# Kernel optimization log

Measured on AMD Instinct MI355X. Metric: run time of the kernel, lower is better.

The kernel has to match this reference:

```python
import jax, jax.numpy as jnp
import numpy as np

N_NODES = 50000
N_HOPS = 4
N_EDGES = 800000
NFEAT = 512
HIDDEN = 512
NCLASS = 128
ATT_HID = 64


def setup_inputs() -> dict:
    key = jax.random.key(0)
    ks = jax.random.split(key, 12)
    s = lambda *sh: 1.0 / np.sqrt(sh[0])
    inp = {}
    inp['x'] = jax.random.normal(ks[0], (N_NODES, NFEAT), dtype=jnp.float32)
    inp['W1'] = jax.random.normal(ks[1], (NFEAT, HIDDEN), dtype=jnp.float32) * s(NFEAT)
    inp['W2'] = jax.random.normal(ks[2], (HIDDEN, NCLASS), dtype=jnp.float32) * s(HIDDEN)
    inp['b2'] = jax.random.normal(ks[3], (NCLASS,), dtype=jnp.float32) * 0.01
    inp['Wg'] = jax.random.normal(ks[4], (NCLASS, NCLASS), dtype=jnp.float32) * s(NCLASS)
    inp['Wa'] = jax.random.normal(ks[5], (2 * NCLASS, ATT_HID), dtype=jnp.float32) * s(2 * NCLASS)
    inp['ba'] = jax.random.normal(ks[6], (ATT_HID,), dtype=jnp.float32) * 0.01
    inp['va'] = jax.random.normal(ks[7], (ATT_HID,), dtype=jnp.float32) * s(ATT_HID)
    inp['adj_values'] = jax.random.uniform(ks[8], (N_HOPS, N_EDGES), dtype=jnp.float32)
    inp['adj_indices'] = jax.random.randint(ks[9], (N_HOPS, 2, N_EDGES), 0, N_NODES, dtype=jnp.int32)
    inp['idx'] = jnp.arange(N_NODES, dtype=jnp.int32)
    return inp


def reference(x, W1, W2, b2, Wg, Wa, ba, va, adj_values, adj_indices, idx):
    # x: [N, nfeat] -> relu(linear1) -> linear2 : [N, C]
    z = jax.nn.relu(x @ W1) @ W2 + b2  # [N, C]
    anchor = z[idx]                    # [Na, C]
    na = idx.shape[0]
    n_hops = adj_indices.shape[0]
    embs = [anchor]
    for h in range(n_hops):  # fixed small structural loop over hops
        rows = adj_indices[h, 0]  # destination anchor row per edge
        cols = adj_indices[h, 1]  # source node per edge
        # sparse matmul: agg[r] = sum_e v_e * z[cols_e]  (LayerConvol)
        agg = jax.ops.segment_sum(adj_values[h][:, None] * z[cols], rows, num_segments=na)
        embs.append(agg @ Wg)  # [Na, C]
    seq = jnp.stack(embs, axis=1)  # [Na, H+1, C]
    # AttenMlp: additive attention of anchor query over hop embeddings
    q = jnp.broadcast_to(anchor[:, None, :], seq.shape)       # [Na, H+1, C]
    feat = jnp.concatenate([q, seq], axis=-1)                 # [Na, H+1, 2C]
    scores = jnp.tanh(feat @ Wa + ba) @ va                    # [Na, H+1]
    alpha = jax.nn.softmax(scores, axis=1)
    out = jnp.einsum('nh,nhc->nc', alpha, seq)                # [Na, C]
    return jax.nn.log_softmax(out, axis=1)
```

## Files before the change

### kernel.cpp

```cpp
#include <hip/hip_runtime.h>

#define NA    50000
#define NFEAT 512
#define HID   512
#define NC    128
#define AH    64
#define NE    800000
#define NHOP  4
#define NBUCK 196
#define CAPB  5120

typedef __bf16 bf16x8 __attribute__((ext_vector_type(8)));
typedef float  f32x4  __attribute__((ext_vector_type(4)));

__device__ __forceinline__ unsigned short f2bf(float f){
  union { float f; unsigned u; } a; a.f = f;
  return (unsigned short)((a.u + 0x7fffu + ((a.u >> 16) & 1u)) >> 16);
}
__device__ __forceinline__ float bf2f(unsigned short h){
  union { unsigned u; float f; } a; a.u = ((unsigned)h) << 16;
  return a.f;
}
__device__ __forceinline__ float uasf(unsigned u){
  union { unsigned u; float f; } a; a.u = u;
  return a.f;
}
__device__ __forceinline__ float tanh_fast(float x){
  x = fminf(15.f, fmaxf(-15.f, x));
  float e = __expf(2.f * x);
  return (e - 1.f) / (e + 1.f);
}

__device__ __forceinline__ void g2l16(const void* g, void* l){
  __builtin_amdgcn_global_load_lds(
      (const __attribute__((address_space(1))) void*)g,
      (__attribute__((address_space(3))) void*)l, 16, 0, 0);
}


__global__ void cast_x_kernel(const float* __restrict__ in, unsigned short* __restrict__ out, int n4){
  int i = blockIdx.x * 256 + threadIdx.x;
  if (i >= n4) return;
  float4 v = reinterpret_cast<const float4*>(in)[i];
  ushort4 o; o.x = f2bf(v.x); o.y = f2bf(v.y); o.z = f2bf(v.z); o.w = f2bf(v.w);
  reinterpret_cast<ushort4*>(out)[i] = o;
}

__global__ void prep_kernel(const float* __restrict__ W1, const float* __restrict__ W2,
                            const float* __restrict__ Wg, const float* __restrict__ Wa,
                            unsigned short* __restrict__ W1T, unsigned short* __restrict__ W2T,
                            unsigned short* __restrict__ WgT, unsigned short* __restrict__ WaT,
                            unsigned short* __restrict__ WfuseT){
  const int b = blockIdx.x, tid = threadIdx.x;
  if (b < 1024){
    int i = b * 256 + tid;
    int n = i >> 9, k = i & 511;
    W1T[i] = f2bf(W1[(size_t)k * HID + n]);
  } else if (b < 1280){
    int i = (b - 1024) * 256 + tid;
    int n = i >> 9, k = i & 511;
    W2T[i] = f2bf(W2[(size_t)k * NC + n]);
  } else if (b < 1344){
    int i = (b - 1280) * 256 + tid;
    int n = i >> 7, k = i & 127;
    WgT[i] = f2bf(Wg[(size_t)k * NC + n]);
  } else if (b < 1408){
    int i = (b - 1344) * 256 + tid;
    int n = i >> 7, k = i & 127;
    float v = (n < 64) ? Wa[(size_t)k * AH + n] : Wa[(size_t)(128 + k) * AH + (n - 64)];
    WaT[i] = f2bf(v);
  } else {
    int i = (b - 1408) * 256 + tid;
    int j = i >> 7, n = i & 127;
    float s = 0.f;
    for (int k = 0; k < 128; k++)
      s += Wa[(size_t)(128 + k) * AH + j] * Wg[(size_t)n * 128 + k];
    WfuseT[i] = f2bf(s);
  }
}

template<int OP, int SWZ>
__global__ __launch_bounds__(256) void gemm_bt(
    const unsigned short* __restrict__ A, const unsigned short* __restrict__ BT,
    unsigned short* __restrict__ Cb, const float* __restrict__ bias,
    int M, int N, int K)
{
  int row0, col0;
  if (SWZ){
    const int xcd = blockIdx.x & 7, slot = blockIdx.x >> 3;
    const int r = xcd * 49 + (slot >> 2);
    if (r >= 391) return;
    row0 = r * 128; col0 = (slot & 3) * 128;
  } else {
    row0 = blockIdx.x * 128; col0 = blockIdx.y * 128;
  }
  __shared__ unsigned short As[128 * 32];
  __shared__ unsigned short Bs[128 * 32];
  const int tid = threadIdx.x;
  const int wave = tid >> 6, lane = tid & 63;
  const int wr = (wave >> 1) * 64, wc = (wave & 1) * 64;
  f32x4 acc[4][4];
  #pragma unroll
  for (int m = 0; m < 4; m++)
    #pragma unroll
    for (int n = 0; n < 4; n++) acc[m][n] = (f32x4){0.f, 0.f, 0.f, 0.f};
  const int lrow = lane >> 2, lk = (lane & 3) * 8;

  for (int k0 = 0; k0 < K; k0 += 32){
    __syncthreads();
    #pragma unroll
    for (int j = 0; j < 2; j++){
      const int rb = (wave * 2 + j) * 16;
      const int ra = rb + lrow;
      int gr = row0 + ra; gr = gr < M ? gr : M - 1;
      g2l16(A + (size_t)gr * K + k0 + lk, As + rb * 32);
      int gc = col0 + ra; gc = gc < N ? gc : N - 1;
      g2l16(BT + (size_t)gc * K + k0 + lk, Bs + rb * 32);
    }
    __syncthreads();
    bf16x8 af[4], bfr[4];
    #pragma unroll
    for (int m = 0; m < 4; m++)
      af[m] = *reinterpret_cast<const bf16x8*>(&As[(wr + m * 16 + (lane & 15)) * 32 + (lane >> 4) * 8]);
    #pragma unroll
    for (int n = 0; n < 4; n++)
      bfr[n] = *reinterpret_cast<const bf16x8*>(&Bs[(wc + n * 16 + (lane & 15)) * 32 + (lane >> 4) * 8]);
    #pragma unroll
    for (int m = 0; m < 4; m++)
      #pragma unroll
      for (int n = 0; n < 4; n++)
        acc[m][n] = __builtin_amdgcn_mfma_f32_16x16x32_bf16(af[m], bfr[n], acc[m][n], 0, 0, 0);
  }

  const int rbase = row0 + wr + (lane >> 4) * 4;
  const int cbase = col0 + wc + (lane & 15);
  #pragma unroll
  for (int m = 0; m < 4; m++){
    #pragma unroll
    for (int n = 0; n < 4; n++){
      const int col = cbase + n * 16;
      #pragma unroll
      for (int i = 0; i < 4; i++){
        const int row = rbase + m * 16 + i;
        if (row < M && col < N){
          float v = acc[m][n][i];
          if (OP == 0){ v = v > 0.f ? v : 0.f; }
          else        { v += bias[col]; }
          Cb[(size_t)row * N + col] = f2bf(v);
        }
      }
    }
  }
}

__global__ __launch_bounds__(256) void gemm_sweep(
    const unsigned short* __restrict__ aggbf, const unsigned short* __restrict__ zbf,
    const unsigned short* __restrict__ WgT, const unsigned short* __restrict__ WfuseT,
    const unsigned short* __restrict__ WaT,
    unsigned short* __restrict__ embs, unsigned short* __restrict__ EW, float* __restrict__ ZW)
{
  const int zi = blockIdx.z;
  const unsigned short* A; const unsigned short* BT;
  unsigned short* Cb = nullptr; float* Cf = nullptr; int N;
  if (zi < 4)      { A = aggbf + (size_t)zi * NA * NC;       BT = WgT;    Cb = embs + (size_t)zi * NA * NC; N = 128; }
  else if (zi < 8) { A = aggbf + (size_t)(zi - 4) * NA * NC; BT = WfuseT; Cb = EW + (size_t)(zi - 4) * NA * AH; N = 64; }
  else             { A = zbf;                                BT = WaT;    Cf = ZW; N = 128; }

  __shared__ unsigned short As[128 * 32];
  __shared__ unsigned short Bs[128 * 32];
  const int tid = threadIdx.x;
  const int wave = tid >> 6, lane = tid & 63;
  const int row0 = blockIdx.x * 128;
  const int wr = (wave >> 1) * 64, wc = (wave & 1) * 64;
  f32x4 acc[4][4];
  #pragma unroll
  for (int m = 0; m < 4; m++)
    #pragma unroll
    for (int n = 0; n < 4; n++) acc[m][n] = (f32x4){0.f, 0.f, 0.f, 0.f};

  for (int k0 = 0; k0 < 128; k0 += 32){
    __syncthreads();
    #pragma unroll
    for (int j = 0; j < 2; j++){
      const int rb = (wave * 2 + j) * 16;
      int gr = row0 + rb + (lane >> 2); gr = gr < NA ? gr : NA - 1;
      g2l16(A + (size_t)gr * 128 + k0 + (lane & 3) * 8, As + rb * 32);
      int gc = rb + (lane >> 2); gc = gc < N ? gc : N - 1;
      g2l16(BT + (size_t)gc * 128 + k0 + (lane & 3) * 8, Bs + rb * 32);
    }
    __syncthreads();
    bf16x8 bfr[4];
    #pragma unroll
    for (int n = 0; n < 4; n++)
      bfr[n] = *reinterpret_cast<const bf16x8*>(&Bs[(wc + n * 16 + (lane & 15)) * 32 + (lane >> 4) * 8]);
    #pragma unroll
    for (int m = 0; m < 4; m++){
      bf16x8 a = *reinterpret_cast<const bf16x8*>(&As[(wr + m * 16 + (lane & 15)) * 32 + (lane >> 4) * 8]);
      #pragma unroll
      for (int n = 0; n < 4; n++)
        acc[m][n] = __builtin_amdgcn_mfma_f32_16x16x32_bf16(a, bfr[n], acc[m][n], 0, 0, 0);
    }
  }

  const int rbase = row0 + wr + (lane >> 4) * 4;
  const int cbase = wc + (lane & 15);
  #pragma unroll
  for (int m = 0; m < 4; m++){
    #pragma unroll
    for (int n = 0; n < 4; n++){
      const int col = cbase + n * 16;
      #pragma unroll
      for (int i = 0; i < 4; i++){
        const int row = rbase + m * 16 + i;
        if (row < NA && col < N){
          float v = acc[m][n][i];
          if (Cf) Cf[(size_t)row * N + col] = v;
          else    Cb[(size_t)row * N + col] = f2bf(v);
        }
      }
    }
  }
}

__global__ __launch_bounds__(256) void binA_kernel(
    const int* __restrict__ adji, const float* __restrict__ adjv,
    int* __restrict__ fill, long long* __restrict__ binned)
{
  const int h = blockIdx.y, tid = threadIdx.x;
  const int e0 = blockIdx.x * 2048;
  __shared__ int lhist[NBUCK], lbase[NBUCK], lfill[NBUCK];
  for (int i = tid; i < NBUCK; i += 256){ lhist[i] = 0; lfill[i] = 0; }
  __syncthreads();
  int rr[8]; unsigned hh[8]; float vv[8];
  #pragma unroll
  for (int k = 0; k < 8; k++){
    int e = e0 + k * 256 + tid;
    bool ok = e < NE;
    int r = ok ? adji[(size_t)h * 2 * NE + e] : -1;
    int c = ok ? adji[(size_t)h * 2 * NE + NE + e] : 0;
    vv[k] = ok ? adjv[(size_t)h * NE + e] : 0.f;
    rr[k] = r;
    hh[k] = ((unsigned)(r & 255) << 17) | (unsigned)c;
    if (ok) atomicAdd(&lhist[r >> 8], 1);
  }
  __syncthreads();
  if (tid < NBUCK) lbase[tid] = atomicAdd(&fill[h * NBUCK + tid], lhist[tid]);
  __syncthreads();
  #pragma unroll
  for (int k = 0; k < 8; k++){
    if (rr[k] >= 0){
      int b = rr[k] >> 8;
      int p = lbase[b] + atomicAdd(&lfill[b], 1);
      if (p < CAPB)
        binned[((size_t)(h * NBUCK + b)) * CAPB + p] =
            ((long long)hh[k] << 32) | (unsigned)__float_as_int(vv[k]);
    }
  }
}

__global__ __launch_bounds__(1024) void bscan_kernel(const int* __restrict__ fill,
                                                     int* __restrict__ bbase, int* __restrict__ offs){
  __shared__ int tmp[1024];
  int tid = threadIdx.x;
  int v = (tid < NHOP * NBUCK) ? fill[tid] : 0;
  tmp[tid] = v; __syncthreads();
  for (int o = 1; o < 1024; o <<= 1){
    int t = (tid >= o) ? tmp[tid - o] : 0;
    __syncthreads();
    tmp[tid] += t;
    __syncthreads();
  }
  if (tid < NHOP * NBUCK) bbase[tid] = tmp[tid] - v;
  if (tid == 0) offs[NHOP * NA] = NHOP * NE;
}

__global__ __launch_bounds__(256) void binB_kernel(
    const int* __restrict__ fill, const int* __restrict__ bbase,
    const long long* __restrict__ binned,
    int* __restrict__ offs, long long* __restrict__ pvc)
{
  const int b = blockIdx.x, h = blockIdx.y, tid = threadIdx.x;
  const int hb = h * NBUCK + b;
  const int cnt = min(fill[hb], CAPB);
  const long long* src = binned + (size_t)hb * CAPB;
  const int gbase = bbase[hb];
  const int rowbase = b << 8;
  const int nrows = min(256, NA - rowbase);
  __shared__ long long sdata[CAPB];
  __shared__ int lhist[256], lpre[256], lfill2[256];
  lhist[tid] = 0; lfill2[tid] = 0;
  __syncthreads();
  for (int p = tid; p < cnt; p += 256)
    atomicAdd(&lhist[(unsigned)(src[p] >> 32) >> 17], 1);
  __syncthreads();
  int v = lhist[tid]; lpre[tid] = v; __syncthreads();
  for (int o = 1; o < 256; o <<= 1){
    int t = (tid >= o) ? lpre[tid - o] : 0;
    __syncthreads();
    lpre[tid] += t;
    __syncthreads();
  }
  int excl = lpre[tid] - v;
  if (tid < nrows) offs[h * NA + rowbase + tid] = gbase + excl;
  lpre[tid] = excl;
  __syncthreads();
  for (int p = tid; p < cnt; p += 256){
    long long rec = src[p];
    unsigned hi = (unsigned)(rec >> 32);
    int lr = hi >> 17;
    long long out = (rec & 0xffffffffLL) | ((long long)(hi & 0x1ffffu) << 32);
    int pos = lpre[lr] + atomicAdd(&lfill2[lr], 1);
    if (pos < CAPB) sdata[pos] = out;
    else            pvc[(size_t)gbase + pos] = out;
  }
  __syncthreads();
  for (int p = tid; p < cnt; p += 256)
    pvc[(size_t)gbase + p] = sdata[p];
}

#define GR 4
__global__ __launch_bounds__(256) void gather_kernel(
    const int* __restrict__ offs, const long long* __restrict__ pvc,
    const unsigned short* __restrict__ zbf, unsigned short* __restrict__ aggbf)
{
  const int h = blockIdx.y;
  const int w = threadIdx.x >> 6, lane = threadIdx.x & 63;
  const int row = blockIdx.x * GR + w;
  const int base = h * NA + row;
  const int s = offs[base], e = offs[base + 1];
  __shared__ alignas(16) long long srec[GR][64];
  const unsigned* z32 = (const unsigned*)zbf;
  const int4* sr2 = (const int4*)&srec[w][0];
  float a0 = 0.f, a1 = 0.f, b0 = 0.f, b1 = 0.f;
  for (int p0 = s; p0 < e; p0 += 64){
    long long r = 0;
    if (p0 + lane < e) r = __builtin_nontemporal_load(&pvc[p0 + lane]);
    srec[w][lane] = r;
    const int quads = (min(64, e - p0) + 3) >> 2;
    #pragma unroll 4
    for (int q = 0; q < quads; q++){
      int4 ra = sr2[2 * q], rb = sr2[2 * q + 1];
      unsigned z0 = z32[((unsigned)ra.y << 6) + lane];
      unsigned z1 = z32[((unsigned)ra.w << 6) + lane];
      unsigned z2 = z32[((unsigned)rb.y << 6) + lane];
      unsigned z3 = z32[((unsigned)rb.w << 6) + lane];
      float v0 = uasf((unsigned)ra.x), v1 = uasf((unsigned)ra.z);
      float v2 = uasf((unsigned)rb.x), v3 = uasf((unsigned)rb.z);
      a0 += v0 * uasf(z0 << 16); a1 += v0 * uasf(z0 & 0xffff0000u);
      b0 += v1 * uasf(z1 << 16); b1 += v1 * uasf(z1 & 0xffff0000u);
      a0 += v2 * uasf(z2 << 16); a1 += v2 * uasf(z2 & 0xffff0000u);
      b0 += v3 * uasf(z3 << 16); b1 += v3 * uasf(z3 & 0xffff0000u);
    }
  }
  ushort2 o; o.x = f2bf(a0 + b0); o.y = f2bf(a1 + b1);
  *reinterpret_cast<ushort2*>(aggbf + (size_t)base * NC + lane * 2) = o;
}

__global__ __launch_bounds__(256) void final_kernel(
    const unsigned short* __restrict__ zbf, const unsigned short* __restrict__ embs,
    const float* __restrict__ ZW, const unsigned short* __restrict__ EW,
    const float* __restrict__ ba, const float* __restrict__ va,
    const int* __restrict__ idx, float* __restrict__ out)
{
  int tid = threadIdx.x, wave = tid >> 6, lane = tid & 63;
  int n = blockIdx.x * 4 + wave;
  if (n >= NA) return;
  int an = idx[n];
  float qa = ZW[(size_t)an * NC + lane] + ba[lane];
  float vaj = va[lane];
  float sc[5];
  {
    float s0 = ZW[(size_t)an * NC + 64 + lane];
    float t = tanh_fast(qa + s0) * vaj;
    #pragma unroll
    for (int o = 32; o; o >>= 1) t += __shfl_xor(t, o);
    sc[0] = t;
  }
  #pragma unroll
  for (int h = 1; h < 5; h++){
    float sh = bf2f(EW[((size_t)(h - 1) * NA + n) * AH + lane]);
    float t = tanh_fast(qa + sh) * vaj;
    #pragma unroll
    for (int o = 32; o; o >>= 1) t += __shfl_xor(t, o);
    sc[h] = t;
  }
  float m = sc[0];
  #pragma unroll
  for (int h = 1; h < 5; h++) m = fmaxf(m, sc[h]);
  float al[5], den = 0.f;
  #pragma unroll
  for (int h = 0; h < 5; h++){ al[h] = __expf(sc[h] - m); den += al[h]; }
  float inv = 1.f / den;
  float o0 = al[0] * bf2f(zbf[(size_t)an * NC + lane]);
  float o1 = al[0] * bf2f(zbf[(size_t)an * NC + 64 + lane]);
  #pragma unroll
  for (int h = 1; h < 5; h++){
    o0 += al[h] * bf2f(embs[((size_t)(h - 1) * NA + n) * NC + lane]);
    o1 += al[h] * bf2f(embs[((size_t)(h - 1) * NA + n) * NC + 64 + lane]);
  }
  o0 *= inv; o1 *= inv;
  float mx = fmaxf(o0, o1);
  #pragma unroll
  for (int o = 32; o; o >>= 1) mx = fmaxf(mx, __shfl_xor(mx, o));
  float se = __expf(o0 - mx) + __expf(o1 - mx);
  #pragma unroll
  for (int o = 32; o; o >>= 1) se += __shfl_xor(se, o);
  float ls = __logf(se);
  out[(size_t)n * NC + lane]      = o0 - mx - ls;
  out[(size_t)n * NC + 64 + lane] = o1 - mx - ls;
}


extern "C" void kernel_launch(void* const* d_in, const int* in_sizes, int n_in,
                              void* d_out, int out_size, void* d_ws, size_t ws_size,
                              hipStream_t stream)
{
  const float* x    = (const float*)d_in[0];
  const float* W1   = (const float*)d_in[1];
  const float* W2   = (const float*)d_in[2];
  const float* b2   = (const float*)d_in[3];
  const float* Wg   = (const float*)d_in[4];
  const float* Wa   = (const float*)d_in[5];
  const float* ba   = (const float*)d_in[6];
  const float* va   = (const float*)d_in[7];
  const float* adjv = (const float*)d_in[8];
  const int*   adji = (const int*)d_in[9];
  const int*   idx  = (const int*)d_in[10];
  float* out = (float*)d_out;
  (void)in_sizes; (void)n_in; (void)out_size; (void)ws_size;

  char* w = (char*)d_ws;
  auto alloc = [&](size_t b) -> char* { char* p = w; w += (b + 255) & ~(size_t)255; return p; };
  unsigned short* Scr1 = (unsigned short*)alloc((size_t)NA * NFEAT * 2);
  unsigned short* Hbuf = (unsigned short*)alloc((size_t)NA * HID * 2);
  unsigned short* W1T  = (unsigned short*)alloc((size_t)HID * NFEAT * 2);
  unsigned short* W2T  = (unsigned short*)alloc((size_t)NC * HID * 2);
  unsigned short* WgT  = (unsigned short*)alloc((size_t)NC * NC * 2);
  unsigned short* WaT  = (unsigned short*)alloc((size_t)NC * NC * 2);
  unsigned short* WfuseT = (unsigned short*)alloc((size_t)AH * NC * 2);
  unsigned short* zbf  = (unsigned short*)alloc((size_t)NA * NC * 2);
  float*          ZW   = (float*)alloc((size_t)NA * NC * 4);
  int* fill  = (int*)alloc((size_t)NHOP * NBUCK * 4);
  int* bbase = (int*)alloc((size_t)NHOP * NBUCK * 4);
  int* offs  = (int*)alloc(((size_t)NHOP * NA + 1) * 4);
  long long* pvc = (long long*)alloc((size_t)NHOP * NE * 8);
  unsigned short* Xbf   = Scr1;
  long long* binned     = (long long*)Scr1;
  unsigned short* embs  = Scr1;
  unsigned short* aggbf = Hbuf;
  unsigned short* EW    = (unsigned short*)pvc;

  cast_x_kernel<<<dim3((NA * NFEAT / 4 + 255) / 256), 256, 0, stream>>>(x, Xbf, NA * NFEAT / 4);
  prep_kernel<<<dim3(1440), 256, 0, stream>>>(W1, W2, Wg, Wa, W1T, W2T, WgT, WaT, WfuseT);

  gemm_bt<0, 1><<<dim3(1568, 1, 1), 256, 0, stream>>>(Xbf, W1T, Hbuf, nullptr, NA, HID, NFEAT);
  gemm_bt<1, 0><<<dim3(391, 1, 1), 256, 0, stream>>>(Hbuf, W2T, zbf, b2, NA, NC, HID);

  hipMemsetAsync(fill, 0, (size_t)NHOP * NBUCK * 4, stream);
  binA_kernel<<<dim3((NE + 2047) / 2048, NHOP), 256, 0, stream>>>(adji, adjv, fill, binned);
  bscan_kernel<<<dim3(1), 1024, 0, stream>>>(fill, bbase, offs);
  binB_kernel<<<dim3(NBUCK, NHOP), 256, 0, stream>>>(fill, bbase, binned, offs, pvc);

  gather_kernel<<<dim3(NA / GR, NHOP), 256, 0, stream>>>(offs, pvc, zbf, aggbf);
  gemm_sweep<<<dim3(391, 1, 9), 256, 0, stream>>>(aggbf, zbf, WgT, WfuseT, WaT, embs, EW, ZW);

  final_kernel<<<dim3(NA / 4), 256, 0, stream>>>(zbf, embs, ZW, EW, ba, va, idx, out);
}
```

Before: 341.2 us.

## Store ZW in bf16, retile EW gemm, premultiply gather indices, fold memset

Several small changes land together. The ZW projection is now stored as bf16 instead of fp32, which halves its write and read traffic. The EW slices of gemm_sweep use 256-row tiles with all waves covering the full 64 columns instead of wasting half the tile, and the source indices in pvc are pre-shifted by 6 so the gather skips a shift per load. The fill memset is folded into prep_kernel to save one launch. The risks are bf16 rounding on the attention scores, and the pre-shift must still fit in the packed 32 bits.

Result: no change. 337.2 us (-1.2%).

```diff
diff --git a/kernel.cpp b/kernel.cpp
--- a/kernel.cpp
+++ b/kernel.cpp
@@ -50,7 +50,7 @@
                             const float* __restrict__ Wg, const float* __restrict__ Wa,
                             unsigned short* __restrict__ W1T, unsigned short* __restrict__ W2T,
                             unsigned short* __restrict__ WgT, unsigned short* __restrict__ WaT,
-                            unsigned short* __restrict__ WfuseT){
+                            unsigned short* __restrict__ WfuseT, int* __restrict__ fill){
   const int b = blockIdx.x, tid = threadIdx.x;
   if (b < 1024){
     int i = b * 256 + tid;
@@ -69,13 +69,16 @@
     int n = i >> 7, k = i & 127;
     float v = (n < 64) ? Wa[(size_t)k * AH + n] : Wa[(size_t)(128 + k) * AH + (n - 64)];
     WaT[i] = f2bf(v);
-  } else {
+  } else if (b < 1440){
     int i = (b - 1408) * 256 + tid;
     int j = i >> 7, n = i & 127;
     float s = 0.f;
     for (int k = 0; k < 128; k++)
       s += Wa[(size_t)(128 + k) * AH + j] * Wg[(size_t)n * 128 + k];
     WfuseT[i] = f2bf(s);
+  } else {
+    int i = (b - 1440) * 256 + tid;
+    if (i < NHOP * NBUCK) fill[i] = 0;
   }
 }
 
@@ -157,36 +160,54 @@
     const unsigned short* __restrict__ aggbf, const unsigned short* __restrict__ zbf,
     const unsigned short* __restrict__ WgT, const unsigned short* __restrict__ WfuseT,
     const unsigned short* __restrict__ WaT,
-    unsigned short* __restrict__ embs, unsigned short* __restrict__ EW, float* __restrict__ ZW)
+    unsigned short* __restrict__ embs, unsigned short* __restrict__ EW,
+    unsigned short* __restrict__ ZWb)
 {
   const int zi = blockIdx.z;
-  const unsigned short* A; const unsigned short* BT;
-  unsigned short* Cb = nullptr; float* Cf = nullptr; int N;
+  const bool ew = (zi >= 4 && zi < 8);
+  const int row0 = blockIdx.x * (ew ? 256 : 128);
+  if (row0 >= NA) return;
+  const unsigned short* A; const unsigned short* BT; unsigned short* Cb; int N;
   if (zi < 4)      { A = aggbf + (size_t)zi * NA * NC;       BT = WgT;    Cb = embs + (size_t)zi * NA * NC; N = 128; }
-  else if (zi < 8) { A = aggbf + (size_t)(zi - 4) * NA * NC; BT = WfuseT; Cb = EW + (size_t)(zi - 4) * NA * AH; N = 64; }
-  else             { A = zbf;                                BT = WaT;    Cf = ZW; N = 128; }
-
-  __shared__ unsigned short As[128 * 32];
+  else if (ew)     { A = aggbf + (size_t)(zi - 4) * NA * NC; BT = WfuseT; Cb = EW + (size_t)(zi - 4) * NA * AH; N = 64; }
+  else             { A = zbf;                                BT = WaT;    Cb = ZWb; N = 128; }
+
+  __shared__ unsigned short As[256 * 32];
   __shared__ unsigned short Bs[128 * 32];
   const int tid = threadIdx.x;
   const int wave = tid >> 6, lane = tid & 63;
-  const int row0 = blockIdx.x * 128;
-  const int wr = (wave >> 1) * 64, wc = (wave & 1) * 64;
+  const int wr = ew ? wave * 64 : (wave >> 1) * 64;
+  const int wc = ew ? 0 : (wave & 1) * 64;
   f32x4 acc[4][4];
   #pragma unroll
   for (int m = 0; m < 4; m++)
     #pragma unroll
     for (int n = 0; n < 4; n++) acc[m][n] = (f32x4){0.f, 0.f, 0.f, 0.f};
+  const int lrow = lane >> 2, lk = (lane & 3) * 8;
 
   for (int k0 = 0; k0 < 128; k0 += 32){
     __syncthreads();
-    #pragma unroll
-    for (int j = 0; j < 2; j++){
-      const int rb = (wave * 2 + j) * 16;
-      int gr = row0 + rb + (lane >> 2); gr = gr < NA ? gr : NA - 1;
-      g2l16(A + (size_t)gr * 128 + k0 + (lane & 3) * 8, As + rb * 32);
-      int gc = rb + (lane >> 2); gc = gc < N ? gc : N - 1;
-      g2l16(BT + (size_t)gc * 128 + k0 + (lane & 3) * 8, Bs + rb * 32);
+    if (ew){
+      #pragma unroll
+      for (int j = 0; j < 4; j++){
+        const int rb = (wave * 4 + j) * 16;
+        int gr = row0 + rb + lrow; gr = gr < NA ? gr : NA - 1;
+        g2l16(A + (size_t)gr * 128 + k0 + lk, As + rb * 32);
+      }
+      {
+        const int rb = wave * 16;
+        int gc = rb + lrow; gc = gc < 64 ? gc : 63;
+        g2l16(BT + (size_t)gc * 128 + k0 + lk, Bs + rb * 32);
+      }
+    } else {
+      #pragma unroll
+      for (int j = 0; j < 2; j++){
+        const int rb = (wave * 2 + j) * 16;
+        int gr = row0 + rb + lrow; gr = gr < NA ? gr : NA - 1;
+        g2l16(A + (size_t)gr * 128 + k0 + lk, As + rb * 32);
+        int gc = rb + lrow; gc = gc < N ? gc : N - 1;
+        g2l16(BT + (size_t)gc * 128 + k0 + lk, Bs + rb * 32);
+      }
     }
     __syncthreads();
     bf16x8 bfr[4];
@@ -212,11 +233,8 @@
       #pragma unroll
       for (int i = 0; i < 4; i++){
         const int row = rbase + m * 16 + i;
-        if (row < NA && col < N){
-          float v = acc[m][n][i];
-          if (Cf) Cf[(size_t)row * N + col] = v;
-          else    Cb[(size_t)row * N + col] = f2bf(v);
-        }
+        if (row < NA && col < N)
+          Cb[(size_t)row * N + col] = f2bf(acc[m][n][i]);
       }
     }
   }
@@ -308,7 +326,7 @@
     long long rec = src[p];
     unsigned hi = (unsigned)(rec >> 32);
     int lr = hi >> 17;
-    long long out = (rec & 0xffffffffLL) | ((long long)(hi & 0x1ffffu) << 32);
+    long long out = (rec & 0xffffffffLL) | ((long long)((hi & 0x1ffffu) << 6) << 32);
     int pos = lpre[lr] + atomicAdd(&lfill2[lr], 1);
     if (pos < CAPB) sdata[pos] = out;
     else            pvc[(size_t)gbase + pos] = out;
@@ -340,10 +358,10 @@
     #pragma unroll 4
     for (int q = 0; q < quads; q++){
       int4 ra = sr2[2 * q], rb = sr2[2 * q + 1];
-      unsigned z0 = z32[((unsigned)ra.y << 6) + lane];
-      unsigned z1 = z32[((unsigned)ra.w << 6) + lane];
-      unsigned z2 = z32[((unsigned)rb.y << 6) + lane];
-      unsigned z3 = z32[((unsigned)rb.w << 6) + lane];
+      unsigned z0 = z32[(unsigned)ra.y + lane];
+      unsigned z1 = z32[(unsigned)ra.w + lane];
+      unsigned z2 = z32[(unsigned)rb.y + lane];
+      unsigned z3 = z32[(unsigned)rb.w + lane];
       float v0 = uasf((unsigned)ra.x), v1 = uasf((unsigned)ra.z);
       float v2 = uasf((unsigned)rb.x), v3 = uasf((unsigned)rb.z);
       a0 += v0 * uasf(z0 << 16); a1 += v0 * uasf(z0 & 0xffff0000u);
@@ -358,7 +376,7 @@
 
 __global__ __launch_bounds__(256) void final_kernel(
     const unsigned short* __restrict__ zbf, const unsigned short* __restrict__ embs,
-    const float* __restrict__ ZW, const unsigned short* __restrict__ EW,
+    const unsigned short* __restrict__ ZWb, const unsigned short* __restrict__ EW,
     const float* __restrict__ ba, const float* __restrict__ va,
     const int* __restrict__ idx, float* __restrict__ out)
 {
@@ -366,11 +384,11 @@
   int n = blockIdx.x * 4 + wave;
   if (n >= NA) return;
   int an = idx[n];
-  float qa = ZW[(size_t)an * NC + lane] + ba[lane];
+  float qa = bf2f(ZWb[(size_t)an * NC + lane]) + ba[lane];
   float vaj = va[lane];
   float sc[5];
   {
-    float s0 = ZW[(size_t)an * NC + 64 + lane];
+    float s0 = bf2f(ZWb[(size_t)an * NC + 64 + lane]);
     float t = tanh_fast(qa + s0) * vaj;
     #pragma unroll
     for (int o = 32; o; o >>= 1) t += __shfl_xor(t, o);
@@ -439,7 +457,7 @@
   unsigned short* WaT  = (unsigned short*)alloc((size_t)NC * NC * 2);
   unsigned short* WfuseT = (unsigned short*)alloc((size_t)AH * NC * 2);
   unsigned short* zbf  = (unsigned short*)alloc((size_t)NA * NC * 2);
-  float*          ZW   = (float*)alloc((size_t)NA * NC * 4);
+  unsigned short* ZWb  = (unsigned short*)alloc((size_t)NA * NC * 2);
   int* fill  = (int*)alloc((size_t)NHOP * NBUCK * 4);
   int* bbase = (int*)alloc((size_t)NHOP * NBUCK * 4);
   int* offs  = (int*)alloc(((size_t)NHOP * NA + 1) * 4);
@@ -451,18 +469,17 @@
   unsigned short* EW    = (unsigned short*)pvc;
 
   cast_x_kernel<<<dim3((NA * NFEAT / 4 + 255) / 256), 256, 0, stream>>>(x, Xbf, NA * NFEAT / 4);
-  prep_kernel<<<dim3(1440), 256, 0, stream>>>(W1, W2, Wg, Wa, W1T, W2T, WgT, WaT, WfuseT);
+  prep_kernel<<<dim3(1444), 256, 0, stream>>>(W1, W2, Wg, Wa, W1T, W2T, WgT, WaT, WfuseT, fill);
 
   gemm_bt<0, 1><<<dim3(1568, 1, 1), 256, 0, stream>>>(Xbf, W1T, Hbuf, nullptr, NA, HID, NFEAT);
   gemm_bt<1, 0><<<dim3(391, 1, 1), 256, 0, stream>>>(Hbuf, W2T, zbf, b2, NA, NC, HID);
 
-  hipMemsetAsync(fill, 0, (size_t)NHOP * NBUCK * 4, stream);
   binA_kernel<<<dim3((NE + 2047) / 2048, NHOP), 256, 0, stream>>>(adji, adjv, fill, binned);
   bscan_kernel<<<dim3(1), 1024, 0, stream>>>(fill, bbase, offs);
   binB_kernel<<<dim3(NBUCK, NHOP), 256, 0, stream>>>(fill, bbase, binned, offs, pvc);
 
   gather_kernel<<<dim3(NA / GR, NHOP), 256, 0, stream>>>(offs, pvc, zbf, aggbf);
-  gemm_sweep<<<dim3(391, 1, 9), 256, 0, stream>>>(aggbf, zbf, WgT, WfuseT, WaT, embs, EW, ZW);
-
-  final_kernel<<<dim3(NA / 4), 256, 0, stream>>>(zbf, embs, ZW, EW, ba, va, idx, out);
-}
+  gemm_sweep<<<dim3(391, 1, 9), 256, 0, stream>>>(aggbf, zbf, WgT, WfuseT, WaT, embs, EW, ZWb);
+
+  final_kernel<<<dim3(NA / 4), 256, 0, stream>>>(zbf, embs, ZWb, EW, ba, va, idx, out);
+}
```
